# Kernel optimization log

Measured on AMD Instinct MI355X. Metric: run time of the kernel, lower is better.

## Reference

```python
import jax, jax.numpy as jnp
import numpy as np

N_CHANNELS = 512
N_HEAD = 8
N_GROUPS = 32
EPS = 1e-5


def setup_inputs() -> dict:
    key = jax.random.key(0)
    ks = jax.random.split(key, 12)
    C = N_CHANNELS
    s = 1.0 / np.sqrt(C)
    return {
        "x": jax.random.normal(ks[0], (16, C, 32, 32), dtype=jnp.float32),
        "gn_w": jnp.ones((C,), jnp.float32),
        "gn_b": jnp.zeros((C,), jnp.float32),
        "conv_w": jax.random.normal(ks[1], (C, C), dtype=jnp.float32) * s,  # 1x1 conv kernel [out,in]
        "conv_b": jnp.zeros((C,), jnp.float32),
        "wq": jax.random.normal(ks[2], (C, C), dtype=jnp.float32) * s,  # torch Linear weight [out,in]
        "bq": jnp.zeros((C,), jnp.float32),
        "wk": jax.random.normal(ks[3], (C, C), dtype=jnp.float32) * s,
        "bk": jnp.zeros((C,), jnp.float32),
        "wv": jax.random.normal(ks[4], (C, C), dtype=jnp.float32) * s,
        "bv": jnp.zeros((C,), jnp.float32),
        "wo": jax.random.normal(ks[5], (C, C), dtype=jnp.float32) * s,
        "bo": jnp.zeros((C,), jnp.float32),
    }


def _group_norm(x, w, b):
    # x: [B, C, H, W]; normalize over channel groups + spatial dims
    B, C, H, W = x.shape
    xg = x.reshape(B, N_GROUPS, C // N_GROUPS, H, W)
    mean = jnp.mean(xg, axis=(2, 3, 4), keepdims=True)
    var = jnp.var(xg, axis=(2, 3, 4), keepdims=True)
    xn = ((xg - mean) * jax.lax.rsqrt(var + EPS)).reshape(B, C, H, W)
    return xn * w[None, :, None, None] + b[None, :, None, None]


def reference(x, gn_w, gn_b, conv_w, conv_b, wq, bq, wk, bk, wv, bv, wo, bo):
    B, C, H, W = x.shape
    nh, dk = N_HEAD, C // N_HEAD
    scale = dk ** -0.5

    xn = _group_norm(x, gn_w, gn_b)
    # 1x1 conv == per-pixel linear over channels
    x1 = jnp.einsum("bchw,oc->bohw", xn, conv_w) + conv_b[None, :, None, None]
    # b c h w -> b (h w) c
    x1 = x1.reshape(B, C, H * W).transpose(0, 2, 1)  # [B, L, C]

    q = x1 @ wq.T + bq
    k = x1 @ wk.T + bk
    v = x1 @ wv.T + bv

    L = H * W
    # b l (n d) -> b n l d
    q = q.reshape(B, L, nh, dk).transpose(0, 2, 1, 3)
    k = k.reshape(B, L, nh, dk).transpose(0, 2, 1, 3)
    v = v.reshape(B, L, nh, dk).transpose(0, 2, 1, 3)

    attn = jnp.einsum("bnid,bnjd->bnij", q, k) * scale
    score = jax.nn.softmax(attn, axis=-1)
    res = jnp.einsum("bnij,bnjd->bnid", score, v)

    # b n l d -> b l (n d)
    res = res.transpose(0, 2, 1, 3).reshape(B, L, C)
    res = res @ wo.T + bo
    # b l c -> b c h w
    res = res.transpose(0, 2, 1).reshape(B, C, H, W)
    return res + x
```

## Files before the change

kernel.cpp:

```cpp
#include <hip/hip_runtime.h>
#include <math.h>

typedef __attribute__((ext_vector_type(4))) float f4;
typedef __attribute__((ext_vector_type(16))) float f16v;
typedef __attribute__((ext_vector_type(8))) short s8;
typedef __attribute__((ext_vector_type(4))) unsigned short u16x4;
typedef unsigned short u16;
typedef unsigned int u32;

constexpr int kB = 16, kC = 512, kL = 1024, kNH = 8, kG = 32;
constexpr float kEps = 1e-5f;
constexpr float kQScale = 0.18033688011112042f;

__device__ __forceinline__ u16 f2bf(float f) {
    union { float f; unsigned u; } c; c.f = f;
    unsigned u = c.u;
    return (u16)((u + 0x7fffu + ((u >> 16) & 1u)) >> 16);
}
__device__ __forceinline__ float bf2f(u16 v) {
    union { u32 u; float f; } c; c.u = (u32)v << 16; return c.f;
}
__device__ __forceinline__ u32 pkbf(float lo, float hi) {
    u32 r;
    asm("v_cvt_pk_bf16_f32 %0, %1, %2" : "=v"(r) : "v"(lo), "v"(hi));
    return r;
}
__device__ __forceinline__ float exp2hw(float x) {
    float r;
    asm("v_exp_f32 %0, %1" : "=v"(r) : "v"(x));
    return r;
}

__device__ __forceinline__ void gload_lds16(const void* g, void* l) {
    __builtin_amdgcn_global_load_lds(
        (const __attribute__((address_space(1))) void*)g,
        (__attribute__((address_space(3))) void*)l, 16, 0, 0);
}

__global__ __launch_bounds__(256)
void prep1_kernel(const float* __restrict__ wq, const float* __restrict__ wk,
                  const float* __restrict__ wv, const float* __restrict__ wo,
                  const float* __restrict__ cw, const float* __restrict__ bq,
                  const float* __restrict__ bk, const float* __restrict__ bv,
                  const float* __restrict__ convb, const float* __restrict__ x,
                  u16* __restrict__ dst, u16* __restrict__ dstT,
                  float* __restrict__ outb, float2* __restrict__ stats)
{
    __shared__ float t[64][65];
    const int tid = threadIdx.x;
    const int bid = blockIdx.x;
    if (bid < 1024) {
        int idx = bid * 256 + tid;
        int m = idx >> 16;
        int r = idx & 65535;
        const float* srcs[4] = {wq, wk, wv, wo};
        float4 v = ((const float4*)srcs[m])[r];
        u16x4 o; o.x = f2bf(v.x); o.y = f2bf(v.y); o.z = f2bf(v.z); o.w = f2bf(v.w);
        ((u16x4*)dst)[idx] = o;
    } else if (bid < 1088) {
        int b2 = bid - 1024;
        const int c0 = (b2 >> 3) * 64, e0 = (b2 & 7) * 64;
        #pragma unroll
        for (int it = 0; it < 4; ++it) {
            int c = it * 16 + (tid >> 4);
            int e4 = (tid & 15) * 4;
            float4 v = *(const float4*)&cw[(size_t)(c0 + c) * kC + e0 + e4];
            t[c][e4 + 0] = v.x; t[c][e4 + 1] = v.y;
            t[c][e4 + 2] = v.z; t[c][e4 + 3] = v.w;
        }
        __syncthreads();
        #pragma unroll
        for (int it = 0; it < 4; ++it) {
            int e = it * 16 + (tid >> 4);
            int c4 = (tid & 15) * 4;
            u16x4 o;
            o.x = f2bf(t[c4 + 0][e]); o.y = f2bf(t[c4 + 1][e]);
            o.z = f2bf(t[c4 + 2][e]); o.w = f2bf(t[c4 + 3][e]);
            *(u16x4*)&dstT[(size_t)(e0 + e) * kC + c0 + c4] = o;
        }
    } else if (bid < 1472) {
        const int o = (bid - 1088) * 4 + (tid >> 6);
        const int lane = tid & 63;
        const float* w; const float* borig; int m2;
        if (o < 512)       { w = wq; borig = bq; m2 = o; }
        else if (o < 1024) { w = wk; borig = bk; m2 = o - 512; }
        else               { w = wv; borig = bv; m2 = o - 1024; }
        const float* wr = w + (size_t)m2 * kC + lane * 8;
        const float* cb = convb + lane * 8;
        float4 a0 = *(const float4*)wr,  a1 = *(const float4*)(wr + 4);
        float4 b0 = *(const float4*)cb,  b1 = *(const float4*)(cb + 4);
        float s = a0.x * b0.x + a0.y * b0.y + a0.z * b0.z + a0.w * b0.w
                + a1.x * b1.x + a1.y * b1.y + a1.z * b1.z + a1.w * b1.w;
        #pragma unroll
        for (int off = 32; off > 0; off >>= 1) s += __shfl_down(s, off);
        if (lane == 0) outb[o] = s + borig[m2];
    } else {
        const int bg = bid - 1472;
        const float4* p = (const float4*)(x + (size_t)bg * (16 * kL));
        float s = 0.f, ss = 0.f;
        for (int i = tid; i < (16 * kL) / 4; i += 256) {
            float4 v = p[i];
            s  += v.x + v.y + v.z + v.w;
            ss += v.x * v.x + v.y * v.y + v.z * v.z + v.w * v.w;
        }
        #pragma unroll
        for (int off = 32; off > 0; off >>= 1) {
            s  += __shfl_down(s, off);
            ss += __shfl_down(ss, off);
        }
        __shared__ float rs[4], rss[4];
        if ((tid & 63) == 0) { rs[tid >> 6] = s; rss[tid >> 6] = ss; }
        __syncthreads();
        if (tid == 0) {
            float S = rs[0] + rs[1] + rs[2] + rs[3];
            float SS = rss[0] + rss[1] + rss[2] + rss[3];
            const float inv_n = 1.f / (float)(16 * kL);
            float mean = S * inv_n;
            float var  = SS * inv_n - mean * mean;
            stats[bg] = make_float2(mean, rsqrtf(var + kEps));
        }
    }
}

__global__ __launch_bounds__(256)
void gn_t_kernel(const float* __restrict__ x, const float2* __restrict__ stats,
                 const float* __restrict__ gnw, const float* __restrict__ gnb,
                 u16* __restrict__ xt)
{
    __shared__ float t[64][65];
    const int tid = threadIdx.x;
    const int b = blockIdx.z, c0 = blockIdx.y * 64, l0 = blockIdx.x * 64;
    const float* xb = x + ((size_t)(b * kC + c0)) * kL + l0;
    #pragma unroll
    for (int it = 0; it < 4; ++it) {
        int c = it * 16 + (tid >> 4);
        int l4i = (tid & 15) * 4;
        float4 v = *(const float4*)&xb[(size_t)c * kL + l4i];
        float2 st = stats[b * kG + ((c0 + c) >> 4)];
        float a  = st.y * gnw[c0 + c];
        float bb = gnb[c0 + c] - st.x * a;
        t[c][l4i + 0] = v.x * a + bb;
        t[c][l4i + 1] = v.y * a + bb;
        t[c][l4i + 2] = v.z * a + bb;
        t[c][l4i + 3] = v.w * a + bb;
    }
    __syncthreads();
    u16* ob = xt + ((size_t)(b * kL + l0)) * kC + c0;
    #pragma unroll
    for (int it = 0; it < 4; ++it) {
        int l = it * 16 + (tid >> 4);
        int c4 = (tid & 15) * 4;
        u16x4 o;
        o.x = f2bf(t[c4 + 0][l]); o.y = f2bf(t[c4 + 1][l]);
        o.z = f2bf(t[c4 + 2][l]); o.w = f2bf(t[c4 + 3][l]);
        *(u16x4*)&ob[(size_t)l * kC + c4] = o;
    }
}

template <int EPI>
__global__ __launch_bounds__(256, 4)
void gemm_mfma(const u16* __restrict__ W, const u16* __restrict__ X,
               const float* __restrict__ bias0,
               u16* __restrict__ o0, u16* __restrict__ o1, u16* __restrict__ o2,
               const float* __restrict__ resid, float* __restrict__ outf)
{
    __shared__ short lds[2][2][128 * 32];
    const int tid = threadIdx.x, lane = tid & 63, w = tid >> 6;
    const int l15 = lane & 15, l4 = lane >> 4;

    int bxi, byi, bb;
    if constexpr (EPI == 3) {
        bxi = blockIdx.x; byi = blockIdx.y; bb = blockIdx.z;
    } else {
        int f = blockIdx.x;
        int xcd = f & 7, i = f >> 3;
        bb = 2 * xcd + (i & 1);
        int j = i >> 1;
        byi = j >> 3; bxi = j & 7;
    }
    const int bm = byi * 128, bn = bxi * 128;
    const u16* Ag = W + (size_t)bm * kC;
    const u16* Bg = X + ((size_t)bb * kL + bn) * kC;
    const int wm = (w >> 1) * 64, wn = (w & 1) * 64;

    f4 acc[4][4] = {};

    size_t ago[2];
    int ldd[2];
    #pragma unroll
    for (int i = 0; i < 2; ++i) {
        int unit = i * 256 + tid;
        int row = unit >> 2, pos = unit & 3;
        ago[i] = (size_t)row * kC + ((pos ^ (row & 3)) << 3);
        ldd[i] = unit * 8;
    }
    auto stage = [&](int kt, int bi) {
        #pragma unroll
        for (int i = 0; i < 2; ++i) {
            gload_lds16(Ag + ago[i] + kt, &lds[bi][0][ldd[i]]);
            gload_lds16(Bg + ago[i] + kt, &lds[bi][1][ldd[i]]);
        }
    };

    int aoff[4], boff[4];
    #pragma unroll
    for (int f = 0; f < 4; ++f) {
        int ra = wm + f * 16 + l15;
        aoff[f] = ra * 32 + ((l4 ^ (ra & 3)) << 3);
        int rb = wn + f * 16 + l15;
        boff[f] = rb * 32 + ((l4 ^ (rb & 3)) << 3);
    }

    stage(0, 0);

    for (int t = 0; t < 16; ++t) {
        const int cur = t & 1;
        if (t < 15) {
            stage((t + 1) * 32, cur ^ 1);
            asm volatile("s_waitcnt vmcnt(4)" ::: "memory");
        } else {
            asm volatile("s_waitcnt vmcnt(0)" ::: "memory");
        }
        __builtin_amdgcn_s_barrier();

        const short* La = &lds[cur][0][0];
        const short* Lb = &lds[cur][1][0];
        s8 af[4], bfr[4];
        #pragma unroll
        for (int f = 0; f < 4; ++f) {
            af[f]  = *(const s8*)(La + aoff[f]);
            bfr[f] = *(const s8*)(Lb + boff[f]);
        }
        __builtin_amdgcn_s_setprio(1);
        #pragma unroll
        for (int fi = 0; fi < 4; ++fi)
            #pragma unroll
            for (int fj = 0; fj < 4; ++fj)
                acc[fi][fj] = __builtin_amdgcn_mfma_f32_16x16x32_bf16(
                    af[fi], bfr[fj], acc[fi][fj], 0, 0, 0);
        __builtin_amdgcn_s_setprio(0);

        __builtin_amdgcn_s_barrier();
    }

    #pragma unroll
    for (int fi = 0; fi < 4; ++fi) {
        const int mb = bm + wm + fi * 16 + 4 * l4;
        if constexpr (EPI == 2) {
            #pragma unroll
            for (int fj = 0; fj < 4; ++fj) {
                const int n = bn + wn + fj * 16 + l15;
                #pragma unroll
                for (int r = 0; r < 4; ++r) {
                    size_t idx = ((size_t)(bb * kC + mb + r)) * kL + n;
                    outf[idx] = acc[fi][fj][r] + bias0[mb + r] + resid[idx];
                }
            }
        } else if constexpr (EPI == 3) {
            #pragma unroll
            for (int fj = 0; fj < 4; ++fj) {
                const int n = bn + wn + fj * 16 + l15;
                #pragma unroll
                for (int r = 0; r < 4; ++r)
                    o0[(size_t)(mb + r) * kC + n] = f2bf(acc[fi][fj][r]);
            }
        } else {
            if (mb < 1024) {
                u16* dst = (mb < 512) ? o0 : o1;
                const int m2 = mb & 511;
                float bs[4] = {bias0[mb], bias0[mb + 1], bias0[mb + 2], bias0[mb + 3]};
                #pragma unroll
                for (int fj = 0; fj < 4; ++fj) {
                    const int n = bn + wn + fj * 16 + l15;
                    u16x4 pk;
                    #pragma unroll
                    for (int r = 0; r < 4; ++r) pk[r] = f2bf(acc[fi][fj][r] + bs[r]);
                    *(u16x4*)&dst[((size_t)(bb * kL + n)) * kC + m2] = pk;
                }
            } else {
                const int m2 = mb - 1024;
                #pragma unroll
                for (int fj = 0; fj < 4; ++fj) {
                    const int n = bn + wn + fj * 16 + l15;
                    #pragma unroll
                    for (int r = 0; r < 4; ++r)
                        o2[((size_t)(bb * kC + m2 + r)) * kL + n] =
                            f2bf(acc[fi][fj][r] + bias0[mb + r]);
                }
            }
        }
    }
}

__global__ __launch_bounds__(512, 4)
void attn_mfma(const u16* __restrict__ q, const u16* __restrict__ k,
               const u16* __restrict__ vt, u16* __restrict__ o)
{
    __shared__ short ldsK[2][32 * 128];
    __shared__ short ldsV[2][32 * 128];

    const int tid = threadIdx.x, lane = tid & 63, w = tid >> 6;
    const int l31 = lane & 31, h5 = lane >> 5;

    const int flat = blockIdx.x;
    const int bh = (flat & 7) * 16 + (flat >> 5);
    const int qt2 = (flat >> 3) & 3;
    const int b = bh >> 3, h = bh & 7;

    const size_t qrow0 = (size_t)b * kL + qt2 * 256 + w * 32;
    const u16* Qh = q + qrow0 * kC + h * 64;
    const u16* Kb = k + ((size_t)b * kL) * kC + h * 64;
    const u16* Vb = vt + ((size_t)b * kC + h * 64) * kL;

    s8 qf[4];
    #pragma unroll
    for (int ks = 0; ks < 4; ++ks) {
        s8 raw = *(const s8*)(Qh + (size_t)l31 * kC + ks * 16 + h5 * 8);
        #pragma unroll
        for (int e = 0; e < 8; e += 2) {
            u32 pk = pkbf(bf2f((u16)raw[e]) * kQScale,
                          bf2f((u16)raw[e + 1]) * kQScale);
            qf[ks][e]     = (short)(pk & 0xffff);
            qf[ks][e + 1] = (short)(pk >> 16);
        }
    }

    const s8 ones = {0x3F80, 0x3F80, 0x3F80, 0x3F80, 0x3F80, 0x3F80, 0x3F80, 0x3F80};

    f16v oacc0 = {}, oacc1 = {};
    f16v lsum = {};

    size_t kgo, vgo;
    int ldd;
    {
        int u_ = tid;
        int row = u_ >> 4, pos = u_ & 15;
        int s = pos ^ (row & 15);
        int jd = row * 2 + (s >> 3);
        int jda = (jd & 51) | ((jd & 4) << 1) | ((jd & 8) >> 1);
        int sub8 = (s & 7) << 3;
        kgo = (size_t)jda * kC + sub8;
        vgo = (size_t)jd * kL + sub8;
        ldd = u_ * 8;
    }
    auto stage = [&](int jt, int bi) {
        gload_lds16(Kb + kgo + (size_t)jt * (64 * kC), &ldsK[bi][ldd]);
        gload_lds16(Vb + vgo + jt * 64,                &ldsV[bi][ldd]);
    };

    const int sbase = (l31 & 1) << 3;
    const int rlo = l31 >> 1;
    int loff[4];
    #pragma unroll
    for (int ks = 0; ks < 4; ++ks) {
        int s_ = sbase | (2 * ks + h5);
        loff[ks] = rlo * 128 + ((s_ ^ (rlo & 15)) << 3);
    }

    stage(0, 0);

    for (int t = 0; t < 16; ++t) {
        const int cur = t & 1;
        asm volatile("s_waitcnt vmcnt(0)" ::: "memory");
        __builtin_amdgcn_s_barrier();
        if (t < 15) stage(t + 1, cur ^ 1);

        const short* Kl = ldsK[cur];
        const short* Vl = ldsV[cur];

        f16v sf0 = {}, sf1 = {};
        __builtin_amdgcn_s_setprio(1);
        #pragma unroll
        for (int ks = 0; ks < 4; ++ks) {
            s8 kf0 = *(const s8*)(Kl + loff[ks]);
            s8 kf1 = *(const s8*)(Kl + loff[ks] + 2048);
            sf0 = __builtin_amdgcn_mfma_f32_32x32x16_bf16(kf0, qf[ks], sf0, 0, 0, 0);
            sf1 = __builtin_amdgcn_mfma_f32_32x32x16_bf16(kf1, qf[ks], sf1, 0, 0, 0);
        }
        __builtin_amdgcn_s_setprio(0);

        #pragma unroll
        for (int r = 0; r < 16; ++r) {
            sf0[r] = exp2hw(sf0[r]);
            sf1[r] = exp2hw(sf1[r]);
        }

        s8 pf[4];
        #pragma unroll
        for (int ks = 0; ks < 4; ++ks) {
            const f16v& pv = (ks < 2) ? sf0 : sf1;
            const int r0 = 8 * (ks & 1);
            union { u32 wd[4]; s8 v; } u;
            u.wd[0] = pkbf(pv[r0 + 0], pv[r0 + 1]);
            u.wd[1] = pkbf(pv[r0 + 2], pv[r0 + 3]);
            u.wd[2] = pkbf(pv[r0 + 4], pv[r0 + 5]);
            u.wd[3] = pkbf(pv[r0 + 6], pv[r0 + 7]);
            pf[ks] = u.v;
        }

        __builtin_amdgcn_s_setprio(1);
        #pragma unroll
        for (int ks = 0; ks < 4; ++ks) {
            lsum = __builtin_amdgcn_mfma_f32_32x32x16_bf16(ones, pf[ks], lsum, 0, 0, 0);
            s8 vf0 = *(const s8*)(Vl + loff[ks]);
            s8 vf1 = *(const s8*)(Vl + loff[ks] + 2048);
            oacc0 = __builtin_amdgcn_mfma_f32_32x32x16_bf16(vf0, pf[ks], oacc0, 0, 0, 0);
            oacc1 = __builtin_amdgcn_mfma_f32_32x32x16_bf16(vf1, pf[ks], oacc1, 0, 0, 0);
        }
        __builtin_amdgcn_s_setprio(0);
    }

    const float inv = 1.0f / lsum[0];
    u16* orow = o + (qrow0 + l31) * kC + h * 64;
    #pragma unroll
    for (int db = 0; db < 2; ++db) {
        const f16v& oa = db ? oacc1 : oacc0;
        #pragma unroll
        for (int g = 0; g < 4; ++g) {
            int d0 = db * 32 + g * 8 + 4 * h5;
            u32 w0 = pkbf(oa[g * 4 + 0] * inv, oa[g * 4 + 1] * inv);
            u32 w1 = pkbf(oa[g * 4 + 2] * inv, oa[g * 4 + 3] * inv);
            u16x4 pk;
            pk[0] = (u16)(w0 & 0xffff); pk[1] = (u16)(w0 >> 16);
            pk[2] = (u16)(w1 & 0xffff); pk[3] = (u16)(w1 >> 16);
            *(u16x4*)&orow[d0] = pk;
        }
    }
}

extern "C" void kernel_launch(void* const* d_in, const int* in_sizes, int n_in,
                              void* d_out, int out_size, void* d_ws, size_t ws_size,
                              hipStream_t stream)
{
    const float* x      = (const float*)d_in[0];
    const float* gn_w   = (const float*)d_in[1];
    const float* gn_b   = (const float*)d_in[2];
    const float* conv_w = (const float*)d_in[3];
    const float* conv_b = (const float*)d_in[4];
    const float* wq     = (const float*)d_in[5];
    const float* bq     = (const float*)d_in[6];
    const float* wk     = (const float*)d_in[7];
    const float* bk     = (const float*)d_in[8];
    const float* wv     = (const float*)d_in[9];
    const float* bv     = (const float*)d_in[10];
    const float* wo     = (const float*)d_in[11];
    const float* bo     = (const float*)d_in[12];
    float* out = (float*)d_out;

    char* ws = (char*)d_ws;
    float2* stats = (float2*)ws;
    u16* wqkvB  = (u16*)(ws + 8192);
    u16* woB    = wqkvB + 786432;
    u16* convwT = woB + 262144;
    u16* wqkvF  = convwT + 262144;
    float* bqkvF = (float*)(wqkvF + 786432);
    const size_t ACT = (size_t)kB * kL * kC;
    u16* xt  = (u16*)(ws + (6 << 20));
    u16* qb  = xt + ACT;
    u16* kb  = qb + ACT;
    u16* vtb = kb + ACT;
    u16* res = xt;

    prep1_kernel<<<1984, 256, 0, stream>>>(wq, wk, wv, wo, conv_w,
                                           bq, bk, bv, conv_b, x,
                                           wqkvB, convwT, bqkvF, stats);
    gemm_mfma<3><<<dim3(4, 12, 1), 256, 0, stream>>>(
        wqkvB, convwT, nullptr, wqkvF, nullptr, nullptr, nullptr, nullptr);
    gn_t_kernel<<<dim3(16, 8, kB), 256, 0, stream>>>(x, stats, gn_w, gn_b, xt);

    gemm_mfma<1><<<1536, 256, 0, stream>>>(
        wqkvF, xt, bqkvF, qb, kb, vtb, nullptr, nullptr);
    attn_mfma<<<dim3(512), 512, 0, stream>>>(qb, kb, vtb, res);
    gemm_mfma<2><<<512, 256, 0, stream>>>(
        woB, res, bo, nullptr, nullptr, nullptr, x, out);
}
```

Before: 129.1 us.

## Double attention KV tile size, compute row sums in VALU, restructure GEMM pipeline

The attention kernel now stages 128 keys per iteration instead of 64, processing two halves per barrier, which halves the barrier and waitcnt count. The softmax denominator is now summed in registers with a cross-half shuffle instead of an extra MFMA against a ones vector, which removes a quarter of the PV-phase MFMAs. The GEMM loop moves to a single-barrier schedule: it waits on all loads, hits the barrier, then issues the next prefetch. That drops the trailing barrier but exposes more load latency. The larger LDS footprint (64 KB per attention block) may reduce occupancy.

```diff
diff --git a/kernel.cpp b/kernel.cpp
--- a/kernel.cpp
+++ b/kernel.cpp
@@ -215,13 +215,9 @@
 
     for (int t = 0; t < 16; ++t) {
         const int cur = t & 1;
-        if (t < 15) {
-            stage((t + 1) * 32, cur ^ 1);
-            asm volatile("s_waitcnt vmcnt(4)" ::: "memory");
-        } else {
-            asm volatile("s_waitcnt vmcnt(0)" ::: "memory");
-        }
+        asm volatile("s_waitcnt vmcnt(0)" ::: "memory");
         __builtin_amdgcn_s_barrier();
+        if (t < 15) stage((t + 1) * 32, cur ^ 1);
 
         const short* La = &lds[cur][0][0];
         const short* Lb = &lds[cur][1][0];
@@ -239,8 +235,6 @@
                 acc[fi][fj] = __builtin_amdgcn_mfma_f32_16x16x32_bf16(
                     af[fi], bfr[fj], acc[fi][fj], 0, 0, 0);
         __builtin_amdgcn_s_setprio(0);
-
-        __builtin_amdgcn_s_barrier();
     }
 
     #pragma unroll
@@ -296,8 +290,8 @@
 void attn_mfma(const u16* __restrict__ q, const u16* __restrict__ k,
                const u16* __restrict__ vt, u16* __restrict__ o)
 {
-    __shared__ short ldsK[2][32 * 128];
-    __shared__ short ldsV[2][32 * 128];
+    __shared__ short ldsK[2][64 * 128];
+    __shared__ short ldsV[2][64 * 128];
 
     const int tid = threadIdx.x, lane = tid & 63, w = tid >> 6;
     const int l31 = lane & 31, h5 = lane >> 5;
@@ -325,27 +319,31 @@
         }
     }
 
-    const s8 ones = {0x3F80, 0x3F80, 0x3F80, 0x3F80, 0x3F80, 0x3F80, 0x3F80, 0x3F80};
-
     f16v oacc0 = {}, oacc1 = {};
-    f16v lsum = {};
-
-    size_t kgo, vgo;
-    int ldd;
-    {
-        int u_ = tid;
+    float ls = 0.f;
+
+    size_t kgo[2], vgo[2];
+    int ldd[2];
+    #pragma unroll
+    for (int i = 0; i < 2; ++i) {
+        int u_ = i * 512 + tid;
         int row = u_ >> 4, pos = u_ & 15;
         int s = pos ^ (row & 15);
+        int sub8 = (s & 7) << 3;
         int jd = row * 2 + (s >> 3);
-        int jda = (jd & 51) | ((jd & 4) << 1) | ((jd & 8) >> 1);
-        int sub8 = (s & 7) << 3;
-        kgo = (size_t)jda * kC + sub8;
-        vgo = (size_t)jd * kL + sub8;
-        ldd = u_ * 8;
-    }
-    auto stage = [&](int jt, int bi) {
-        gload_lds16(Kb + kgo + (size_t)jt * (64 * kC), &ldsK[bi][ldd]);
-        gload_lds16(Vb + vgo + jt * 64,                &ldsV[bi][ldd]);
+        int jda = (jd & 0x73) | ((jd & 4) << 1) | ((jd & 8) >> 1);
+        kgo[i] = (size_t)jda * kC + sub8;
+        int half = row >> 5, rr = row & 31;
+        int d = rr * 2 + (s >> 3);
+        vgo[i] = (size_t)d * kL + half * 64 + sub8;
+        ldd[i] = u_ * 8;
+    }
+    auto stage = [&](int jt2, int bi) {
+        #pragma unroll
+        for (int i = 0; i < 2; ++i) {
+            gload_lds16(Kb + kgo[i] + (size_t)jt2 * (128 * kC), &ldsK[bi][ldd[i]]);
+            gload_lds16(Vb + vgo[i] + jt2 * 128,                &ldsV[bi][ldd[i]]);
+        }
     };
 
     const int sbase = (l31 & 1) << 3;
@@ -359,58 +357,75 @@
 
     stage(0, 0);
 
-    for (int t = 0; t < 16; ++t) {
+    for (int t = 0; t < 8; ++t) {
         const int cur = t & 1;
         asm volatile("s_waitcnt vmcnt(0)" ::: "memory");
         __builtin_amdgcn_s_barrier();
-        if (t < 15) stage(t + 1, cur ^ 1);
-
-        const short* Kl = ldsK[cur];
-        const short* Vl = ldsV[cur];
-
-        f16v sf0 = {}, sf1 = {};
-        __builtin_amdgcn_s_setprio(1);
-        #pragma unroll
-        for (int ks = 0; ks < 4; ++ks) {
-            s8 kf0 = *(const s8*)(Kl + loff[ks]);
-            s8 kf1 = *(const s8*)(Kl + loff[ks] + 2048);
-            sf0 = __builtin_amdgcn_mfma_f32_32x32x16_bf16(kf0, qf[ks], sf0, 0, 0, 0);
-            sf1 = __builtin_amdgcn_mfma_f32_32x32x16_bf16(kf1, qf[ks], sf1, 0, 0, 0);
-        }
-        __builtin_amdgcn_s_setprio(0);
-
-        #pragma unroll
-        for (int r = 0; r < 16; ++r) {
-            sf0[r] = exp2hw(sf0[r]);
-            sf1[r] = exp2hw(sf1[r]);
-        }
-
-        s8 pf[4];
-        #pragma unroll
-        for (int ks = 0; ks < 4; ++ks) {
-            const f16v& pv = (ks < 2) ? sf0 : sf1;
-            const int r0 = 8 * (ks & 1);
-            union { u32 wd[4]; s8 v; } u;
-            u.wd[0] = pkbf(pv[r0 + 0], pv[r0 + 1]);
-            u.wd[1] = pkbf(pv[r0 + 2], pv[r0 + 3]);
-            u.wd[2] = pkbf(pv[r0 + 4], pv[r0 + 5]);
-            u.wd[3] = pkbf(pv[r0 + 6], pv[r0 + 7]);
-            pf[ks] = u.v;
-        }
-
-        __builtin_amdgcn_s_setprio(1);
-        #pragma unroll
-        for (int ks = 0; ks < 4; ++ks) {
-            lsum = __builtin_amdgcn_mfma_f32_32x32x16_bf16(ones, pf[ks], lsum, 0, 0, 0);
-            s8 vf0 = *(const s8*)(Vl + loff[ks]);
-            s8 vf1 = *(const s8*)(Vl + loff[ks] + 2048);
-            oacc0 = __builtin_amdgcn_mfma_f32_32x32x16_bf16(vf0, pf[ks], oacc0, 0, 0, 0);
-            oacc1 = __builtin_amdgcn_mfma_f32_32x32x16_bf16(vf1, pf[ks], oacc1, 0, 0, 0);
-        }
-        __builtin_amdgcn_s_setprio(0);
-    }
-
-    const float inv = 1.0f / lsum[0];
+        if (t < 7) stage(t + 1, cur ^ 1);
+
+        #pragma unroll
+        for (int half = 0; half < 2; ++half) {
+            const short* Kl = &ldsK[cur][half * 4096];
+            const short* Vl = &ldsV[cur][half * 4096];
+
+            f16v sf0 = {}, sf1 = {};
+            __builtin_amdgcn_s_setprio(1);
+            #pragma unroll
+            for (int ks = 0; ks < 4; ++ks) {
+                s8 kf0 = *(const s8*)(Kl + loff[ks]);
+                s8 kf1 = *(const s8*)(Kl + loff[ks] + 2048);
+                sf0 = __builtin_amdgcn_mfma_f32_32x32x16_bf16(kf0, qf[ks], sf0, 0, 0, 0);
+                sf1 = __builtin_amdgcn_mfma_f32_32x32x16_bf16(kf1, qf[ks], sf1, 0, 0, 0);
+            }
+            __builtin_amdgcn_s_setprio(0);
+
+            #pragma unroll
+            for (int r = 0; r < 16; ++r) {
+                sf0[r] = exp2hw(sf0[r]);
+                sf1[r] = exp2hw(sf1[r]);
+            }
+
+            {
+                float t0 = 0.f, t1 = 0.f, t2 = 0.f, t3 = 0.f;
+                #pragma unroll
+                for (int r = 0; r < 16; r += 4) {
+                    t0 += sf0[r];     t1 += sf0[r + 1];
+                    t2 += sf0[r + 2]; t3 += sf0[r + 3];
+                }
+                #pragma unroll
+                for (int r = 0; r < 16; r += 4) {
+                    t0 += sf1[r];     t1 += sf1[r + 1];
+                    t2 += sf1[r + 2]; t3 += sf1[r + 3];
+                }
+                ls += (t0 + t1) + (t2 + t3);
+            }
+
+            s8 pf[4];
+            #pragma unroll
+            for (int ks = 0; ks < 4; ++ks) {
+                const f16v& pv = (ks < 2) ? sf0 : sf1;
+                const int r0 = 8 * (ks & 1);
+                union { u32 wd[4]; s8 v; } u;
+                u.wd[0] = pkbf(pv[r0 + 0], pv[r0 + 1]);
+                u.wd[1] = pkbf(pv[r0 + 2], pv[r0 + 3]);
+                u.wd[2] = pkbf(pv[r0 + 4], pv[r0 + 5]);
+                u.wd[3] = pkbf(pv[r0 + 6], pv[r0 + 7]);
+                pf[ks] = u.v;
+            }
+
+            __builtin_amdgcn_s_setprio(1);
+            #pragma unroll
+            for (int ks = 0; ks < 4; ++ks) {
+                s8 vf0 = *(const s8*)(Vl + loff[ks]);
+                s8 vf1 = *(const s8*)(Vl + loff[ks] + 2048);
+                oacc0 = __builtin_amdgcn_mfma_f32_32x32x16_bf16(vf0, pf[ks], oacc0, 0, 0, 0);
+                oacc1 = __builtin_amdgcn_mfma_f32_32x32x16_bf16(vf1, pf[ks], oacc1, 0, 0, 0);
+            }
+            __builtin_amdgcn_s_setprio(0);
+        }
+    }
+
+    const float inv = 1.0f / (ls + __shfl_xor(ls, 32));
     u16* orow = o + (qrow0 + l31) * kC + h * 64;
     #pragma unroll
     for (int db = 0; db < 2; ++db) {
```

Result: slower. 186.1 us (+44.2%).
